# Performance work log

Hardware: AMD Instinct MI355X
Metric: run time of the kernel (lower is better)

Reference implementation:

```python
import jax, jax.numpy as jnp
import numpy as np

N_NODES = 100000


def _gcn_conv(x, edge_index, W, b, n):
    """PyG GCNConv: h = x @ W; add self-loops; symmetric deg^-1/2 norm; scatter-add; + b."""
    h = x @ W                                            # [N, F_out]
    src = jnp.concatenate([edge_index[0], jnp.arange(n)])  # self-loops appended
    dst = jnp.concatenate([edge_index[1], jnp.arange(n)])
    deg = jax.ops.segment_sum(jnp.ones_like(dst, dtype=h.dtype), dst, num_segments=n)
    dinv = jnp.where(deg > 0, jax.lax.rsqrt(deg), 0.0)   # deg^-1/2 with inf->0
    norm = dinv[src] * dinv[dst]                         # [E+N]
    msg = h[src] * norm[:, None]                         # gather + scale
    out = jax.ops.segment_sum(msg, dst, num_segments=n)  # scatter-add
    return out + b


def setup_inputs() -> dict:
    key = jax.random.key(0)
    ks = jax.random.split(key, 4)
    x = jax.random.normal(ks[0], (N_NODES, 128), dtype=jnp.float32)
    edge_index = jax.random.randint(ks[1], (2, 1600000), 0, N_NODES, dtype=jnp.int64)
    W1 = jax.random.normal(ks[2], (128, 128), dtype=jnp.float32) * (1.0 / np.sqrt(128))
    b1 = jnp.zeros((128,), dtype=jnp.float32)
    W2 = jax.random.normal(ks[3], (128, 16), dtype=jnp.float32) * (1.0 / np.sqrt(128))
    b2 = jnp.zeros((16,), dtype=jnp.float32)
    return {"x": x, "edge_index": edge_index, "W1": W1, "b1": b1, "W2": W2, "b2": b2}


def reference(x, edge_index, W1, b1, W2, b2):
    n = x.shape[0]
    h = jax.nn.relu(_gcn_conv(x, edge_index, W1, b1, n))
    out = _gcn_conv(h, edge_index, W2, b2, n)
    return out
```

## Files before the change

kernel.cpp:

```cpp
#include <hip/hip_runtime.h>
#include <hip/hip_bf16.h>

typedef __attribute__((ext_vector_type(8))) short bf16x8;
typedef __attribute__((ext_vector_type(4))) float f32x4;
typedef __attribute__((ext_vector_type(8))) unsigned short u16x8;

#define ELL_W 64
#define BSH   7
#define BMSK  ((1 << BSH) - 1)
#define BCAP  2432
#define CHUNK 4096


__device__ __forceinline__ float bf2f(unsigned short u) {
    return __uint_as_float(((unsigned int)u) << 16);
}
__device__ __forceinline__ unsigned short f2bf(float f) {
    unsigned int u = __float_as_uint(f);
    unsigned int r = (u + 0x7fffu + ((u >> 16) & 1u)) >> 16;
    return (unsigned short)r;
}
__device__ __forceinline__ int sel4(int sub, int4 v) {
    int s = (sub & 1) ? v.y : v.x;
    int t = (sub & 1) ? v.w : v.z;
    return (sub & 2) ? t : s;
}


__global__ void setup_kernel(int N, int NB, int* __restrict__ gcur,
                             const float* __restrict__ W1, unsigned short* __restrict__ wfrag,
                             unsigned short* __restrict__ h1, unsigned short* __restrict__ h2) {
    int nb2 = (NB * 16 + 255) >> 8;
    int b = blockIdx.x;
    if (b < nb2) {
        int i = b * 256 + threadIdx.x;
        if (i < NB * 16) gcur[i] = 0;
    } else if (b < nb2 + 8) {
        int t = (b - nb2) * 256 + threadIdx.x;
        if (t < 2048) {
            int ln = t & 63;
            int blk = t >> 6;
            int j = blk >> 2, k0 = blk & 3;
            int nn = ln & 15, cc = ln >> 4;
            int n = j * 16 + nn;
            unsigned short tmp[8];
#pragma unroll
            for (int i = 0; i < 8; ++i) {
                int k = k0 * 32 + cc * 8 + i;
                tmp[i] = f2bf(W1[(size_t)k * 128 + n]);
            }
            *(uint4*)&wfrag[(size_t)t * 8] = *(const uint4*)tmp;
        }
    } else {
        if (threadIdx.x < 128) h1[(size_t)N * 128 + threadIdx.x] = 0;
        if (threadIdx.x < 16) h2[(size_t)N * 16 + threadIdx.x] = 0;
    }
}


__global__ __launch_bounds__(256) void p1_partition_kernel(const int* __restrict__ ei, int E, int N, int NB,
                                                           int* __restrict__ gcur, int* __restrict__ bucket) {
    __shared__ int hist[1024];
    __shared__ int gbase[1024];
    __shared__ int cur2[1024];
    int tid = threadIdx.x;
    int c0 = blockIdx.x * CHUNK;

    for (int i = tid; i < NB; i += 256) { hist[i] = 0; cur2[i] = 0; }
    __syncthreads();

    int rec[16], bkt[16];
#pragma unroll
    for (int k = 0; k < 16; ++k) {
        int e = c0 + k * 256 + tid;
        int b = -1, r = 0;
        if (e < E) {
            int s = ei[e], d = ei[E + e];
            if ((unsigned)s < (unsigned)N && (unsigned)d < (unsigned)N) {
                b = d >> BSH;
                r = (s << BSH) | (d & BMSK);
            }
        }
        bkt[k] = b; rec[k] = r;
        if (b >= 0) atomicAdd(&hist[b], 1);
    }
    __syncthreads();

    for (int i = tid; i < NB; i += 256) {
        int c = hist[i];
        gbase[i] = (c > 0) ? atomicAdd(&gcur[i * 16], c) : 0;
    }
    __syncthreads();

#pragma unroll
    for (int k = 0; k < 16; ++k) {
        int b = bkt[k];
        if (b >= 0) {
            int r = atomicAdd(&cur2[b], 1);
            int pos = gbase[b] + r;
            if (pos < BCAP) bucket[(size_t)b * BCAP + pos] = rec[k];
        }
    }
}


__global__ __launch_bounds__(256) void p2_ell_kernel(const int* __restrict__ bucket,
                                                     const int* __restrict__ gcur, int N,
                                                     int* __restrict__ deg, float* __restrict__ dinv,
                                                     int* __restrict__ ell) {
    __shared__ int lcur[128];
    int b = blockIdx.x;
    if (threadIdx.x < 128) lcur[threadIdx.x] = 0;
    __syncthreads();

    int cnt = gcur[b * 16]; if (cnt > BCAP) cnt = BCAP;
    const int* reg = &bucket[(size_t)b * BCAP];
    for (int k = threadIdx.x; k < cnt; k += 256) {
        int rec = reg[k];
        int s = (int)(((unsigned)rec) >> BSH);
        int dloc = rec & BMSK;
        int pos = atomicAdd(&lcur[dloc], 1);
        if (pos < ELL_W) ell[((size_t)(b << BSH) + dloc) * ELL_W + pos] = s;
    }
    __syncthreads();

    if (threadIdx.x < 128) {
        int i = (b << BSH) + threadIdx.x;
        if (i < N) {
            int d = lcur[threadIdx.x];
            deg[i] = d;
            dinv[i] = rsqrtf((float)(d + 1));
            if (d > ELL_W) d = ELL_W;
            int d8 = (d + 7) & ~7; if (d8 > ELL_W) d8 = ELL_W;
            for (int k = d; k < d8; ++k) ell[(size_t)i * ELL_W + k] = N;
        }
    }
}


__global__ __launch_bounds__(256) void gemm1_mfma_kernel(const float* __restrict__ X,
                                                         const unsigned short* __restrict__ wfrag,
                                                         const float* __restrict__ dinv,
                                                         unsigned short* __restrict__ H, int N) {
    __shared__ __align__(16) unsigned short wl[16384];
    int tid = threadIdx.x;
    {
        uint4* dst = (uint4*)wl;
        const uint4* src = (const uint4*)wfrag;
        for (int idx = tid; idx < 2048; idx += 256) dst[idx] = src[idx];
    }
    __syncthreads();

    int lane = tid & 63;
    int wave = tid >> 6;
    int m0 = blockIdx.x * 128 + wave * 32;
    int mrow = lane & 15;
    int kc = lane >> 4;

    f32x4 acc[2][8];
#pragma unroll
    for (int rt = 0; rt < 2; ++rt)
#pragma unroll
        for (int j = 0; j < 8; ++j) acc[rt][j] = (f32x4)(0.f);

#pragma unroll
    for (int k0 = 0; k0 < 4; ++k0) {
        bf16x8 a[2];
#pragma unroll
        for (int rt = 0; rt < 2; ++rt) {
            int row = m0 + rt * 16 + mrow;
            bf16x8 av = (bf16x8)(short)0;
            if (row < N) {
                const float4* p = (const float4*)&X[(size_t)row * 128 + k0 * 32 + kc * 8];
                float4 v0 = p[0], v1 = p[1];
                av[0] = (short)f2bf(v0.x); av[1] = (short)f2bf(v0.y);
                av[2] = (short)f2bf(v0.z); av[3] = (short)f2bf(v0.w);
                av[4] = (short)f2bf(v1.x); av[5] = (short)f2bf(v1.y);
                av[6] = (short)f2bf(v1.z); av[7] = (short)f2bf(v1.w);
            }
            a[rt] = av;
        }
#pragma unroll
        for (int j = 0; j < 8; ++j) {
            bf16x8 b = *(const bf16x8*)&wl[((size_t)(j * 4 + k0) * 64 + lane) * 8];
            acc[0][j] = __builtin_amdgcn_mfma_f32_16x16x32_bf16(a[0], b, acc[0][j], 0, 0, 0);
            acc[1][j] = __builtin_amdgcn_mfma_f32_16x16x32_bf16(a[1], b, acc[1][j], 0, 0, 0);
        }
    }

#pragma unroll
    for (int rt = 0; rt < 2; ++rt) {
#pragma unroll
        for (int r = 0; r < 4; ++r) {
            int row = m0 + rt * 16 + 4 * kc + r;
            if (row < N) {
                float dv = dinv[row];
#pragma unroll
                for (int j = 0; j < 8; ++j) {
                    H[(size_t)row * 128 + j * 16 + mrow] = f2bf(dv * acc[rt][j][r]);
                }
            }
        }
    }
}


__global__ __launch_bounds__(256) void agg128_fused_kernel(const unsigned short* __restrict__ H,
                                                           const int* __restrict__ ell,
                                                           const int* __restrict__ deg,
                                                           const float* __restrict__ dinv,
                                                           const float* __restrict__ b1,
                                                           const float* __restrict__ W2,
                                                           unsigned short* __restrict__ h2out, int N) {
    __shared__ float gbuf[4][128];
    int lane = threadIdx.x & 63;
    int w = threadIdx.x >> 6;
    int i0 = blockIdx.x * 16 + w * 4;

    int n = lane & 15;
    int q = lane >> 4;
    int sub = lane >> 4;
    int fl = lane & 15;

    float w2r[32];
#pragma unroll
    for (int m = 0; m < 32; ++m) {
        int mm = (m + 8 * q) & 31;
        w2r[m] = W2[(size_t)(q * 32 + mm) * 16 + n];
    }

    for (int nn = 0; nn < 4; ++nn) {
        int i = i0 + nn;
        if (i >= N) break;
        int d = deg[i]; if (d > ELL_W) d = ELL_W;
        int d8 = (d + 7) & ~7; if (d8 > ELL_W) d8 = ELL_W;
        float di = dinv[i];

        float a0, a1, a2, a3, a4, a5, a6, a7;
        {
            u16x8 hv = *(const u16x8*)&H[(size_t)i * 128 + 8 * fl];
            bool z = (sub != 0);
            a0 = z ? 0.f : bf2f(hv[0]); a1 = z ? 0.f : bf2f(hv[1]);
            a2 = z ? 0.f : bf2f(hv[2]); a3 = z ? 0.f : bf2f(hv[3]);
            a4 = z ? 0.f : bf2f(hv[4]); a5 = z ? 0.f : bf2f(hv[5]);
            a6 = z ? 0.f : bf2f(hv[6]); a7 = z ? 0.f : bf2f(hv[7]);
        }

        const int* row = &ell[(size_t)i * ELL_W];
        for (int e = 0; e < d8; e += 8) {
            int4 svA = *(const int4*)&row[e];
            int4 svB = *(const int4*)&row[e + 4];
            int sA = sel4(sub, svA);
            int sB = sel4(sub, svB);
            u16x8 gA = *(const u16x8*)&H[(size_t)sA * 128 + 8 * fl];
            u16x8 gB = *(const u16x8*)&H[(size_t)sB * 128 + 8 * fl];
            a0 += bf2f(gA[0]) + bf2f(gB[0]);
            a1 += bf2f(gA[1]) + bf2f(gB[1]);
            a2 += bf2f(gA[2]) + bf2f(gB[2]);
            a3 += bf2f(gA[3]) + bf2f(gB[3]);
            a4 += bf2f(gA[4]) + bf2f(gB[4]);
            a5 += bf2f(gA[5]) + bf2f(gB[5]);
            a6 += bf2f(gA[6]) + bf2f(gB[6]);
            a7 += bf2f(gA[7]) + bf2f(gB[7]);
        }

        a0 += __shfl_xor(a0, 32, 64); a0 += __shfl_xor(a0, 16, 64);
        a1 += __shfl_xor(a1, 32, 64); a1 += __shfl_xor(a1, 16, 64);
        a2 += __shfl_xor(a2, 32, 64); a2 += __shfl_xor(a2, 16, 64);
        a3 += __shfl_xor(a3, 32, 64); a3 += __shfl_xor(a3, 16, 64);
        a4 += __shfl_xor(a4, 32, 64); a4 += __shfl_xor(a4, 16, 64);
        a5 += __shfl_xor(a5, 32, 64); a5 += __shfl_xor(a5, 16, 64);
        a6 += __shfl_xor(a6, 32, 64); a6 += __shfl_xor(a6, 16, 64);
        a7 += __shfl_xor(a7, 32, 64); a7 += __shfl_xor(a7, 16, 64);

        if (sub == 0) {
            float4 bb0 = *(const float4*)&b1[8 * fl];
            float4 bb1 = *(const float4*)&b1[8 * fl + 4];
            float4 g0, g1;
            g0.x = fmaxf(di * a0 + bb0.x, 0.f);
            g0.y = fmaxf(di * a1 + bb0.y, 0.f);
            g0.z = fmaxf(di * a2 + bb0.z, 0.f);
            g0.w = fmaxf(di * a3 + bb0.w, 0.f);
            g1.x = fmaxf(di * a4 + bb1.x, 0.f);
            g1.y = fmaxf(di * a5 + bb1.y, 0.f);
            g1.z = fmaxf(di * a6 + bb1.z, 0.f);
            g1.w = fmaxf(di * a7 + bb1.w, 0.f);
            *(float4*)&gbuf[w][8 * fl] = g0;
            *(float4*)&gbuf[w][8 * fl + 4] = g1;
        }
        asm volatile("s_waitcnt lgkmcnt(0)" ::: "memory");

        float partial = 0.f;
#pragma unroll
        for (int t = 0; t < 8; ++t) {
            int off = (t * 4 + 8 * q) & 31;
            float4 gv = *(const float4*)&gbuf[w][q * 32 + off];
            partial += gv.x * w2r[t * 4 + 0] + gv.y * w2r[t * 4 + 1] +
                       gv.z * w2r[t * 4 + 2] + gv.w * w2r[t * 4 + 3];
        }
        partial += __shfl_xor(partial, 16, 64);
        partial += __shfl_xor(partial, 32, 64);
        if (lane < 16) h2out[(size_t)i * 16 + lane] = f2bf(di * partial);
    }
}


__global__ __launch_bounds__(256) void agg16_kernel(const unsigned short* __restrict__ H,
                                                    const int* __restrict__ ell,
                                                    const int* __restrict__ deg,
                                                    const float* __restrict__ dinv,
                                                    const float* __restrict__ b2,
                                                    float* __restrict__ out, int N) {
    int lane = threadIdx.x & 63;
    int i = blockIdx.x * 4 + (threadIdx.x >> 6);
    if (i >= N) return;
    int fl = lane & 7;
    int sub = lane >> 3;

    int d = deg[i]; if (d > ELL_W) d = ELL_W;
    int d8 = (d + 7) & ~7; if (d8 > ELL_W) d8 = ELL_W;
    float di = dinv[i];
    const int* row = &ell[(size_t)i * ELL_W];

    float a0, a1;
    {
        ushort2 hv = *(const ushort2*)&H[(size_t)i * 16 + 2 * fl];
        bool z = (sub != 0);
        a0 = z ? 0.f : bf2f(hv.x);
        a1 = z ? 0.f : bf2f(hv.y);
    }

    for (int e = 0; e < d8; e += 8) {
        int4 svA = *(const int4*)&row[e];
        int4 svB = *(const int4*)&row[e + 4];
        int sA_ = sel4(sub & 3, svA);
        int sB_ = sel4(sub & 3, svB);
        int s = (sub & 4) ? sB_ : sA_;
        ushort2 g = *(const ushort2*)&H[(size_t)s * 16 + 2 * fl];
        a0 += bf2f(g.x);
        a1 += bf2f(g.y);
    }

    a0 += __shfl_xor(a0, 32, 64); a0 += __shfl_xor(a0, 16, 64); a0 += __shfl_xor(a0, 8, 64);
    a1 += __shfl_xor(a1, 32, 64); a1 += __shfl_xor(a1, 16, 64); a1 += __shfl_xor(a1, 8, 64);

    if (lane < 8) {
        float2 o;
        o.x = di * a0 + b2[2 * fl];
        o.y = di * a1 + b2[2 * fl + 1];
        *(float2*)&out[(size_t)i * 16 + 2 * fl] = o;
    }
}


extern "C" void kernel_launch(void* const* d_in, const int* in_sizes, int n_in,
                              void* d_out, int out_size, void* d_ws, size_t ws_size,
                              hipStream_t stream) {
    const float* x = (const float*)d_in[0];
    const int* ei = (const int*)d_in[1];
    const float* W1 = (const float*)d_in[2];
    const float* b1 = (const float*)d_in[3];
    const float* W2 = (const float*)d_in[4];
    const float* b2 = (const float*)d_in[5];
    float* out = (float*)d_out;

    const int N = in_sizes[0] / 128;
    const int E = in_sizes[1] / 2;
    const int NB = (N + BMSK) >> BSH;

    char* base = (char*)d_ws;
    size_t off = 0;
    auto align_up = [](size_t v) { return (v + 255) & ~(size_t)255; };

    int* deg = (int*)(base + off);                         off = align_up(off + (size_t)N * 4);
    float* dinv = (float*)(base + off);                    off = align_up(off + (size_t)N * 4);
    int* ell = (int*)(base + off);                         off = align_up(off + (size_t)N * ELL_W * 4);
    int* gcur = (int*)(base + off);                        off = align_up(off + (size_t)NB * 16 * 4);
    int* bucket = (int*)(base + off);                      off = align_up(off + (size_t)NB * BCAP * 4);
    unsigned short* wfrag = (unsigned short*)(base + off); off = align_up(off + (size_t)16384 * 2);
    unsigned short* h1 = (unsigned short*)(base + off);    off = align_up(off + (size_t)(N + 1) * 128 * 2);
    unsigned short* h2 = (unsigned short*)(base + off);    off = align_up(off + (size_t)(N + 1) * 16 * 2);

    int nb2 = (NB * 16 + 255) >> 8;
    setup_kernel<<<nb2 + 9, 256, 0, stream>>>(N, NB, gcur, W1, wfrag, h1, h2);

    int nchunks = (E + CHUNK - 1) / CHUNK;
    p1_partition_kernel<<<nchunks, 256, 0, stream>>>(ei, E, N, NB, gcur, bucket);
    p2_ell_kernel<<<NB, 256, 0, stream>>>(bucket, gcur, N, deg, dinv, ell);

    gemm1_mfma_kernel<<<(N + 127) / 128, 256, 0, stream>>>(x, wfrag, dinv, h1, N);
    agg128_fused_kernel<<<(N + 15) / 16, 256, 0, stream>>>(h1, ell, deg, dinv, b1, W2, h2, N);
    agg16_kernel<<<(N + 3) / 4, 256, 0, stream>>>(h2, ell, deg, dinv, b2, out, N);
}
```

Measured before the change: 192.1 us.

## Slice H1 feature-major so layer-1 aggregation gathers from cache-resident slices

GEMM1 now writes H1 in a transposed layout of eight 16-feature slices, each stored contiguously per node. The fused aggregate-plus-W2 kernel is split into a per-slice aggregation kernel, indexed by blockIdx, and a separate small GEMM2 kernel. Each slice of H1 is 3.2 MB, so random neighbor gathers within a slice can stay resident in L2 or the infinity cache instead of touching the full 25 MB H1. The cost is an extra kernel launch and an extra intermediate buffer G1T that must be written and read back, and the edge-index rows are now reread once per slice. The agg16 kernel index selection is also simplified to a direct load.

```diff
diff --git a/kernel.cpp b/kernel.cpp
--- a/kernel.cpp
+++ b/kernel.cpp
@@ -29,7 +29,7 @@
 
 __global__ void setup_kernel(int N, int NB, int* __restrict__ gcur,
                              const float* __restrict__ W1, unsigned short* __restrict__ wfrag,
-                             unsigned short* __restrict__ h1, unsigned short* __restrict__ h2) {
+                             unsigned short* __restrict__ h1T, unsigned short* __restrict__ h2) {
     int nb2 = (NB * 16 + 255) >> 8;
     int b = blockIdx.x;
     if (b < nb2) {
@@ -52,7 +52,10 @@
             *(uint4*)&wfrag[(size_t)t * 8] = *(const uint4*)tmp;
         }
     } else {
-        if (threadIdx.x < 128) h1[(size_t)N * 128 + threadIdx.x] = 0;
+        if (threadIdx.x < 128) {
+            int s = threadIdx.x >> 4, f = threadIdx.x & 15;
+            h1T[((size_t)s * (N + 1) + N) * 16 + f] = 0;
+        }
         if (threadIdx.x < 16) h2[(size_t)N * 16 + threadIdx.x] = 0;
     }
 }
@@ -141,7 +144,7 @@
 __global__ __launch_bounds__(256) void gemm1_mfma_kernel(const float* __restrict__ X,
                                                          const unsigned short* __restrict__ wfrag,
                                                          const float* __restrict__ dinv,
-                                                         unsigned short* __restrict__ H, int N) {
+                                                         unsigned short* __restrict__ H1T, int N) {
     __shared__ __align__(16) unsigned short wl[16384];
     int tid = threadIdx.x;
     {
@@ -197,7 +200,7 @@
                 float dv = dinv[row];
 #pragma unroll
                 for (int j = 0; j < 8; ++j) {
-                    H[(size_t)row * 128 + j * 16 + mrow] = f2bf(dv * acc[rt][j][r]);
+                    H1T[((size_t)j * (N + 1) + row) * 16 + mrow] = f2bf(dv * acc[rt][j][r]);
                 }
             }
         }
@@ -205,103 +208,95 @@
 }
 
 
-__global__ __launch_bounds__(256) void agg128_fused_kernel(const unsigned short* __restrict__ H,
-                                                           const int* __restrict__ ell,
-                                                           const int* __restrict__ deg,
-                                                           const float* __restrict__ dinv,
-                                                           const float* __restrict__ b1,
-                                                           const float* __restrict__ W2,
-                                                           unsigned short* __restrict__ h2out, int N) {
-    __shared__ float gbuf[4][128];
+__global__ __launch_bounds__(256) void agg_slice_kernel(const unsigned short* __restrict__ H1T,
+                                                        const int* __restrict__ ell,
+                                                        const int* __restrict__ deg,
+                                                        const float* __restrict__ dinv,
+                                                        const float* __restrict__ b1,
+                                                        unsigned short* __restrict__ G1T,
+                                                        int N) {
+    int s = blockIdx.x & 7;
+    int grp = blockIdx.x >> 3;
     int lane = threadIdx.x & 63;
     int w = threadIdx.x >> 6;
-    int i0 = blockIdx.x * 16 + w * 4;
-
-    int n = lane & 15;
-    int q = lane >> 4;
-    int sub = lane >> 4;
-    int fl = lane & 15;
-
-    float w2r[32];
-#pragma unroll
-    for (int m = 0; m < 32; ++m) {
-        int mm = (m + 8 * q) & 31;
-        w2r[m] = W2[(size_t)(q * 32 + mm) * 16 + n];
-    }
-
+    int es = lane >> 3;
+    int fp = lane & 7;
+
+    const unsigned short* Hs = H1T + (size_t)s * (N + 1) * 16;
+    unsigned short* Gs = G1T + (size_t)s * N * 16;
+    float bx = b1[s * 16 + 2 * fp];
+    float by = b1[s * 16 + 2 * fp + 1];
+
+    int ibase = grp * 16 + w * 4;
+#pragma unroll
     for (int nn = 0; nn < 4; ++nn) {
-        int i = i0 + nn;
-        if (i >= N) break;
+        int i = ibase + nn;
+        if (i >= N) continue;
         int d = deg[i]; if (d > ELL_W) d = ELL_W;
         int d8 = (d + 7) & ~7; if (d8 > ELL_W) d8 = ELL_W;
         float di = dinv[i];
 
-        float a0, a1, a2, a3, a4, a5, a6, a7;
-        {
-            u16x8 hv = *(const u16x8*)&H[(size_t)i * 128 + 8 * fl];
-            bool z = (sub != 0);
-            a0 = z ? 0.f : bf2f(hv[0]); a1 = z ? 0.f : bf2f(hv[1]);
-            a2 = z ? 0.f : bf2f(hv[2]); a3 = z ? 0.f : bf2f(hv[3]);
-            a4 = z ? 0.f : bf2f(hv[4]); a5 = z ? 0.f : bf2f(hv[5]);
-            a6 = z ? 0.f : bf2f(hv[6]); a7 = z ? 0.f : bf2f(hv[7]);
-        }
+        ushort2 hv = *(const ushort2*)&Hs[(unsigned)i * 16u + 2u * (unsigned)fp];
+        float a0 = (es == 0) ? bf2f(hv.x) : 0.f;
+        float a1 = (es == 0) ? bf2f(hv.y) : 0.f;
 
         const int* row = &ell[(size_t)i * ELL_W];
         for (int e = 0; e < d8; e += 8) {
-            int4 svA = *(const int4*)&row[e];
-            int4 svB = *(const int4*)&row[e + 4];
-            int sA = sel4(sub, svA);
-            int sB = sel4(sub, svB);
-            u16x8 gA = *(const u16x8*)&H[(size_t)sA * 128 + 8 * fl];
-            u16x8 gB = *(const u16x8*)&H[(size_t)sB * 128 + 8 * fl];
-            a0 += bf2f(gA[0]) + bf2f(gB[0]);
-            a1 += bf2f(gA[1]) + bf2f(gB[1]);
-            a2 += bf2f(gA[2]) + bf2f(gB[2]);
-            a3 += bf2f(gA[3]) + bf2f(gB[3]);
-            a4 += bf2f(gA[4]) + bf2f(gB[4]);
-            a5 += bf2f(gA[5]) + bf2f(gB[5]);
-            a6 += bf2f(gA[6]) + bf2f(gB[6]);
-            a7 += bf2f(gA[7]) + bf2f(gB[7]);
-        }
-
-        a0 += __shfl_xor(a0, 32, 64); a0 += __shfl_xor(a0, 16, 64);
-        a1 += __shfl_xor(a1, 32, 64); a1 += __shfl_xor(a1, 16, 64);
-        a2 += __shfl_xor(a2, 32, 64); a2 += __shfl_xor(a2, 16, 64);
-        a3 += __shfl_xor(a3, 32, 64); a3 += __shfl_xor(a3, 16, 64);
-        a4 += __shfl_xor(a4, 32, 64); a4 += __shfl_xor(a4, 16, 64);
-        a5 += __shfl_xor(a5, 32, 64); a5 += __shfl_xor(a5, 16, 64);
-        a6 += __shfl_xor(a6, 32, 64); a6 += __shfl_xor(a6, 16, 64);
-        a7 += __shfl_xor(a7, 32, 64); a7 += __shfl_xor(a7, 16, 64);
-
-        if (sub == 0) {
-            float4 bb0 = *(const float4*)&b1[8 * fl];
-            float4 bb1 = *(const float4*)&b1[8 * fl + 4];
-            float4 g0, g1;
-            g0.x = fmaxf(di * a0 + bb0.x, 0.f);
-            g0.y = fmaxf(di * a1 + bb0.y, 0.f);
-            g0.z = fmaxf(di * a2 + bb0.z, 0.f);
-            g0.w = fmaxf(di * a3 + bb0.w, 0.f);
-            g1.x = fmaxf(di * a4 + bb1.x, 0.f);
-            g1.y = fmaxf(di * a5 + bb1.y, 0.f);
-            g1.z = fmaxf(di * a6 + bb1.z, 0.f);
-            g1.w = fmaxf(di * a7 + bb1.w, 0.f);
-            *(float4*)&gbuf[w][8 * fl] = g0;
-            *(float4*)&gbuf[w][8 * fl + 4] = g1;
-        }
-        asm volatile("s_waitcnt lgkmcnt(0)" ::: "memory");
-
-        float partial = 0.f;
-#pragma unroll
-        for (int t = 0; t < 8; ++t) {
-            int off = (t * 4 + 8 * q) & 31;
-            float4 gv = *(const float4*)&gbuf[w][q * 32 + off];
-            partial += gv.x * w2r[t * 4 + 0] + gv.y * w2r[t * 4 + 1] +
-                       gv.z * w2r[t * 4 + 2] + gv.w * w2r[t * 4 + 3];
-        }
-        partial += __shfl_xor(partial, 16, 64);
-        partial += __shfl_xor(partial, 32, 64);
-        if (lane < 16) h2out[(size_t)i * 16 + lane] = f2bf(di * partial);
-    }
+            int idx = __builtin_nontemporal_load(&row[e + es]);
+            ushort2 g = *(const ushort2*)&Hs[(unsigned)idx * 16u + 2u * (unsigned)fp];
+            a0 += bf2f(g.x);
+            a1 += bf2f(g.y);
+        }
+        a0 += __shfl_xor(a0, 8, 64);
+        a0 += __shfl_xor(a0, 16, 64);
+        a0 += __shfl_xor(a0, 32, 64);
+        a1 += __shfl_xor(a1, 8, 64);
+        a1 += __shfl_xor(a1, 16, 64);
+        a1 += __shfl_xor(a1, 32, 64);
+
+        if (es == 0) {
+            unsigned short ox = f2bf(fmaxf(di * a0 + bx, 0.f));
+            unsigned short oy = f2bf(fmaxf(di * a1 + by, 0.f));
+            unsigned int packed = (unsigned int)ox | ((unsigned int)oy << 16);
+            __builtin_nontemporal_store(packed, (unsigned int*)&Gs[(unsigned)i * 16u + 2u * (unsigned)fp]);
+        }
+    }
+}
+
+
+__global__ __launch_bounds__(256) void gemm2_kernel(const unsigned short* __restrict__ G1T,
+                                                    const float* __restrict__ W2,
+                                                    const float* __restrict__ dinv,
+                                                    unsigned short* __restrict__ h2out, int N) {
+    __shared__ float W2l[128][16];
+    int tid = threadIdx.x;
+    for (int idx = tid; idx < 2048; idx += 256) W2l[idx >> 4][idx & 15] = W2[idx];
+    __syncthreads();
+
+    int r = tid >> 2;
+    int cg = tid & 3;
+    int i = blockIdx.x * 64 + r;
+    if (i >= N) return;
+
+    u16x8 xr[16];
+#pragma unroll
+    for (int s = 0; s < 8; ++s) {
+        const uint4* p = (const uint4*)&G1T[((size_t)s * N + i) * 16];
+        *(uint4*)&xr[s * 2] = p[0];
+        *(uint4*)&xr[s * 2 + 1] = p[1];
+    }
+    float di = dinv[i];
+
+    float a0 = 0.f, a1 = 0.f, a2 = 0.f, a3 = 0.f;
+    const unsigned short* xs = (const unsigned short*)xr;
+#pragma unroll
+    for (int k = 0; k < 128; ++k) {
+        float xv = bf2f(xs[k]);
+        float4 wv = *(const float4*)&W2l[k][cg * 4];
+        a0 += xv * wv.x; a1 += xv * wv.y; a2 += xv * wv.z; a3 += xv * wv.w;
+    }
+    unsigned short o[4] = { f2bf(di * a0), f2bf(di * a1), f2bf(di * a2), f2bf(di * a3) };
+    *(uint2*)&h2out[(size_t)i * 16 + cg * 4] = *(const uint2*)o;
 }
 
 
@@ -331,11 +326,7 @@
     }
 
     for (int e = 0; e < d8; e += 8) {
-        int4 svA = *(const int4*)&row[e];
-        int4 svB = *(const int4*)&row[e + 4];
-        int sA_ = sel4(sub & 3, svA);
-        int sB_ = sel4(sub & 3, svB);
-        int s = (sub & 4) ? sB_ : sA_;
+        int s = row[e + sub];
         ushort2 g = *(const ushort2*)&H[(size_t)s * 16 + 2 * fl];
         a0 += bf2f(g.x);
         a1 += bf2f(g.y);
@@ -378,17 +369,21 @@
     int* gcur = (int*)(base + off);                        off = align_up(off + (size_t)NB * 16 * 4);
     int* bucket = (int*)(base + off);                      off = align_up(off + (size_t)NB * BCAP * 4);
     unsigned short* wfrag = (unsigned short*)(base + off); off = align_up(off + (size_t)16384 * 2);
-    unsigned short* h1 = (unsigned short*)(base + off);    off = align_up(off + (size_t)(N + 1) * 128 * 2);
+    unsigned short* h1T = (unsigned short*)(base + off);   off = align_up(off + (size_t)8 * (N + 1) * 16 * 2);
+    unsigned short* g1T = (unsigned short*)(base + off);   off = align_up(off + (size_t)8 * N * 16 * 2);
     unsigned short* h2 = (unsigned short*)(base + off);    off = align_up(off + (size_t)(N + 1) * 16 * 2);
 
     int nb2 = (NB * 16 + 255) >> 8;
-    setup_kernel<<<nb2 + 9, 256, 0, stream>>>(N, NB, gcur, W1, wfrag, h1, h2);
+    setup_kernel<<<nb2 + 9, 256, 0, stream>>>(N, NB, gcur, W1, wfrag, h1T, h2);
 
     int nchunks = (E + CHUNK - 1) / CHUNK;
     p1_partition_kernel<<<nchunks, 256, 0, stream>>>(ei, E, N, NB, gcur, bucket);
     p2_ell_kernel<<<NB, 256, 0, stream>>>(bucket, gcur, N, deg, dinv, ell);
 
-    gemm1_mfma_kernel<<<(N + 127) / 128, 256, 0, stream>>>(x, wfrag, dinv, h1, N);
-    agg128_fused_kernel<<<(N + 15) / 16, 256, 0, stream>>>(h1, ell, deg, dinv, b1, W2, h2, N);
+    gemm1_mfma_kernel<<<(N + 127) / 128, 256, 0, stream>>>(x, wfrag, dinv, h1T, N);
+
+    int ngrp = (N + 15) / 16;
+    agg_slice_kernel<<<ngrp * 8, 256, 0, stream>>>(h1T, ell, deg, dinv, b1, g1T, N);
+    gemm2_kernel<<<(N + 63) / 64, 256, 0, stream>>>(g1T, W2, dinv, h2, N);
     agg16_kernel<<<(N + 3) / 4, 256, 0, stream>>>(h2, ell, deg, dinv, b2, out, N);
 }
```

New measurement: 411.4 us. 2.14x slower.
